# Kernel optimization log

Measured on AMD Instinct MI355X. Metric: run time of the kernel, lower is better.

Reference implementation:

```python
import jax, jax.numpy as jnp
import numpy as np

L, B, D, H = 128, 4, 768, 300
NT, NR = 7, 12  # ner tags, relation types
EPS = 1e-5


def _cummax(v):
    # torch: cumsum(softmax(v, -1), -1)
    return jnp.cumsum(jax.nn.softmax(v, axis=-1), axis=-1)


def _layernorm(v, g, b):
    mu = jnp.mean(v, axis=-1, keepdims=True)
    var = jnp.var(v, axis=-1, keepdims=True)
    return (v - mu) * jax.lax.rsqrt(var + EPS) * g + b


def setup_inputs() -> dict:
    key = jax.random.key(0)
    ks = jax.random.split(key, 24)
    s = lambda fan_in: 1.0 / np.sqrt(fan_in)
    u = lambda k, shape, sc: jax.random.uniform(k, shape, jnp.float32, -sc, sc)
    inp = {
        "x": jax.random.normal(ks[0], (L, B, D), jnp.float32),
        "mask": jnp.ones((L, B), jnp.float32),
        # PFN_Unit
        "W_ih": u(ks[1], (5 * H, D), s(D)), "b_ih": u(ks[2], (5 * H,), s(D)),
        "W_hh": u(ks[3], (5 * H, H), s(H)), "b_hh": u(ks[4], (5 * H,), s(H)),
        "W_tr": u(ks[5], (H, 3 * H), s(3 * H)), "b_tr": u(ks[6], (H,), s(3 * H)),
        # NERUnit
        "n_W": u(ks[7], (H, 2 * H), s(2 * H)), "n_b": u(ks[8], (H,), s(2 * H)),
        "ner_hW": u(ks[9], (H, 3 * H), s(3 * H)), "ner_hb": u(ks[10], (H,), s(3 * H)),
        "ner_g": jnp.ones((H,), jnp.float32), "ner_beta": jnp.zeros((H,), jnp.float32),
        "ner_tW": u(ks[11], (NT, H), s(H)), "ner_tb": u(ks[12], (NT,), s(H)),
        # ReUnit
        "r_W": u(ks[13], (H, 2 * H), s(2 * H)), "r_b": u(ks[14], (H,), s(2 * H)),
        "re_hW": u(ks[15], (H, 3 * H), s(3 * H)), "re_hb": u(ks[16], (H,), s(3 * H)),
        "re_g": jnp.ones((H,), jnp.float32), "re_beta": jnp.zeros((H,), jnp.float32),
        "re_tW": u(ks[17], (NR, H), s(H)), "re_tb": u(ks[18], (NR,), s(H)),
    }
    return inp


def _encoder(x, W_ih, b_ih, W_hh, b_hh, W_tr, b_tr):
    pre = jnp.einsum('lbd,gd->lbg', x, W_ih) + b_ih  # precompute input transform [L,B,5H]

    def step(carry, gx):
        h, c_in = carry
        gates = gx + h @ W_hh.T + b_hh
        c, eg_cin, rg_cin, eg_c, rg_c = jnp.split(gates, 5, axis=1)
        eg_cin, rg_cin = 1.0 - _cummax(eg_cin), _cummax(rg_cin)
        eg_c, rg_c = 1.0 - _cummax(eg_c), _cummax(rg_c)
        c = jnp.tanh(c)
        ov_c = rg_c * eg_c
        up_c, dn_c = rg_c - ov_c, eg_c - ov_c
        ov_i = rg_cin * eg_cin
        up_i, dn_i = rg_cin - ov_i, eg_cin - ov_i
        share = ov_i * c_in + ov_c * c
        c_re = up_i * c_in + up_c * c + share
        c_ner = dn_i * c_in + dn_c * c + share
        c_out = jnp.concatenate([c_re, c_ner, share], axis=-1) @ W_tr.T + b_tr
        h_out = jnp.tanh(c_out)
        return (h_out, c_out), (jnp.tanh(c_ner), jnp.tanh(c_re), jnp.tanh(share))

    h0 = jnp.zeros((x.shape[1], W_hh.shape[1]), x.dtype)
    _, (h_ner, h_re, h_share) = jax.lax.scan(step, (h0, h0), pre)
    return h_ner, h_re, h_share  # each [L,B,H]


def _pair_unit(h_task, h_share, mask, gW, gb, hW, hb, ln_g, ln_b, tW, tb, diag):
    length = h_task.shape[0]
    # global feature: tanh(Linear(cat(share, task))), max over time
    h_glob = jnp.tanh(jnp.concatenate([h_share, h_task], axis=-1) @ gW.T + gb)  # [L,B,H]
    g = jnp.max(h_glob, axis=0)  # [B,H]
    # pairwise feature [L,L,B,3H] = cat(start, end, global)
    st = jnp.broadcast_to(h_task[:, None], (length, length) + h_task.shape[1:])
    en = jnp.broadcast_to(h_task[None, :], (length, length) + h_task.shape[1:])
    gb4 = jnp.broadcast_to(g, (length, length) + g.shape)
    feat = jnp.concatenate([st, en, gb4], axis=-1)
    out = _layernorm(feat @ hW.T + hb, ln_g, ln_b)
    out = jax.nn.elu(out)  # eval mode: dropout is identity
    out = jax.nn.sigmoid(out @ tW.T + tb)  # [L,L,B,T]
    # mask
    m = mask[:, None, :] * mask[None, :, :]  # [L,L,B]
    if diag:
        m = m * jnp.triu(jnp.ones((length, length), out.dtype))[:, :, None]
    return out * m[..., None]


def reference(x, mask, W_ih, b_ih, W_hh, b_hh, W_tr, b_tr,
              n_W, n_b, ner_hW, ner_hb, ner_g, ner_beta, ner_tW, ner_tb,
              r_W, r_b, re_hW, re_hb, re_g, re_beta, re_tW, re_tb):
    h_ner, h_re, h_share = _encoder(x, W_ih, b_ih, W_hh, b_hh, W_tr, b_tr)
    ner = _pair_unit(h_ner, h_share, mask, n_W, n_b, ner_hW, ner_hb,
                     ner_g, ner_beta, ner_tW, ner_tb, diag=True)
    re = _pair_unit(h_re, h_share, mask, r_W, r_b, re_hW, re_hb,
                    re_g, re_beta, re_tW, re_tb, diag=False)
    return ner, re
```

## Files before the change

kernel.cpp:

```cpp
#include <hip/hip_runtime.h>

#define LLEN 128
#define BB 4
#define DD 768
#define HH 300
#define G5 1500
#define H3 900
#define NTT 7
#define NRR 12
#define NCHB 10
#define RPB 150
#define OPB 30

#define C_WIH  0
#define C_X    1152000
#define C_WHH2 1545216
#define C_WTR2 1995216
#define F_BIH  2265216
#define F_BTR  2266720
#define F_PRE  2267040
#define F_HG0  (F_PRE)
#define F_HG1  (F_PRE+153600)
#define F_A0   (F_PRE+307200)
#define F_E0   (F_PRE+460800)
#define F_GF0  (F_PRE+616832)
#define F_GF1  (F_PRE+618048)
#define F_HNER (F_PRE+768000)
#define F_HRE  (F_HNER+153600)
#define F_HSH  (F_HRE+153600)
#define F_A1   0
#define F_E1   153600
#define F_AUX  (F_HSH+153600)
#define AUXB   2432
#define AUX_FL 9728
#define WS_NEED_BYTES ((size_t)(F_AUX+11776)*4)

typedef unsigned short u16;
typedef unsigned int u32;
typedef float f4 __attribute__((ext_vector_type(4)));
typedef int i4 __attribute__((ext_vector_type(4)));

__device__ __forceinline__ float bf2f(u16 u) {
  union { u32 i; float f; } v; v.i = ((u32)u) << 16; return v.f;
}
__device__ __forceinline__ u16 f2bf(float f) {
  union { float f; u32 i; } v; v.f = f;
  u32 r = v.i + 0x7fffu + ((v.i >> 16) & 1u);
  return (u16)(r >> 16);
}
__device__ __forceinline__ float ldin(const void* p, int i, bool f32) {
  return f32 ? ((const float*)p)[i] : bf2f(((const u16*)p)[i]);
}
__device__ __forceinline__ bool is32(const void* mk) {
  return ((const u16*)mk)[0] == 0;
}
__device__ __forceinline__ float wsum(float x) {
  #pragma unroll
  for (int d = 1; d < 64; d <<= 1) x += __shfl_xor(x, d);
  return x;
}
__device__ __forceinline__ void astore(float* p, float v) {
  union { float f; int i; } u; u.f = v;
  __hip_atomic_store((int*)p, u.i, __ATOMIC_RELAXED, __HIP_MEMORY_SCOPE_AGENT);
}
__device__ __forceinline__ void gbar(int* flag, int tid, int target) {
  __syncthreads();
  if (tid == 0) {
    __builtin_amdgcn_s_waitcnt(0);
    __hip_atomic_fetch_add(flag, 1, __ATOMIC_RELAXED, __HIP_MEMORY_SCOPE_AGENT);
    int it = 0;
    while (__hip_atomic_load(flag, __ATOMIC_RELAXED, __HIP_MEMORY_SCOPE_AGENT) < target) {
      __builtin_amdgcn_s_sleep(1);
      if (++it > 50000) break;
    }
  }
  __syncthreads();
}
__device__ __forceinline__ f4 ld4x(const f4* p, int mode) {
  f4 v;
  if (mode)
    asm volatile("global_load_dwordx4 %0, %1, off sc0\n\ts_waitcnt vmcnt(0)"
                 : "=v"(v) : "v"(p) : "memory");
  else
    asm volatile("global_load_dwordx4 %0, %1, off sc0 sc1\n\ts_waitcnt vmcnt(0)"
                 : "=v"(v) : "v"(p) : "memory");
  return v;
}
__device__ __forceinline__ float ld1x(const float* p, int mode) {
  float v;
  if (mode)
    asm volatile("global_load_dword %0, %1, off sc0\n\ts_waitcnt vmcnt(0)"
                 : "=v"(v) : "v"(p) : "memory");
  else
    asm volatile("global_load_dword %0, %1, off sc0 sc1\n\ts_waitcnt vmcnt(0)"
                 : "=v"(v) : "v"(p) : "memory");
  return v;
}
__device__ __forceinline__ int ldix(const int* p, int mode) {
  int v;
  if (mode)
    asm volatile("global_load_dword %0, %1, off sc0\n\ts_waitcnt vmcnt(0)"
                 : "=v"(v) : "v"(p) : "memory");
  else
    asm volatile("global_load_dword %0, %1, off sc0 sc1\n\ts_waitcnt vmcnt(0)"
                 : "=v"(v) : "v"(p) : "memory");
  return v;
}
__device__ __forceinline__ void exst(float* p, float v, int mode) {
  if (mode) *p = v; else astore(p, v);
}
__device__ __forceinline__ int poll10(const int* slots, int tok, int mode) {
  i4 a, b, c;
  if (mode)
    asm volatile("global_load_dwordx4 %0, %3, off sc0\n\t"
                 "global_load_dwordx4 %1, %4, off sc0\n\t"
                 "global_load_dwordx4 %2, %5, off sc0\n\t"
                 "s_waitcnt vmcnt(0)"
                 : "=&v"(a), "=&v"(b), "=&v"(c)
                 : "v"(slots), "v"(slots + 4), "v"(slots + 8) : "memory");
  else
    asm volatile("global_load_dwordx4 %0, %3, off sc0 sc1\n\t"
                 "global_load_dwordx4 %1, %4, off sc0 sc1\n\t"
                 "global_load_dwordx4 %2, %5, off sc0 sc1\n\t"
                 "s_waitcnt vmcnt(0)"
                 : "=&v"(a), "=&v"(b), "=&v"(c)
                 : "v"(slots), "v"(slots + 4), "v"(slots + 8) : "memory");
  return (a.x >= tok) & (a.y >= tok) & (a.z >= tok) & (a.w >= tok) &
         (b.x >= tok) & (b.y >= tok) & (b.z >= tok) & (b.w >= tok) &
         (c.x >= tok) & (c.y >= tok);
}
__device__ __forceinline__ void sbar(int* slots, int ch, int tok, int tid, int mode) {
  asm volatile("s_waitcnt vmcnt(0)" ::: "memory");
  __syncthreads();
  if (tid == 0) {
    if (mode) slots[ch] = tok;
    else __hip_atomic_store(slots + ch, tok, __ATOMIC_RELAXED, __HIP_MEMORY_SCOPE_AGENT);
  }
  if (tid < 64) {
    int it = 0;
    while (!poll10(slots, tok, mode)) {
      __builtin_amdgcn_s_sleep(1);
      if (++it > 5000) break;
    }
  }
  __syncthreads();
}
__device__ __forceinline__ int claim_bc(int* cl, int nb) {
  unsigned xcd;
  asm volatile("s_getreg_b32 %0, hwreg(HW_REG_XCC_ID)" : "=s"(xcd));
  xcd &= 7u;
  int rank = __hip_atomic_fetch_add(cl + xcd, 1, __ATOMIC_RELAXED, __HIP_MEMORY_SCOPE_AGENT);
  __hip_atomic_fetch_add(cl + 8, 1, __ATOMIC_RELAXED, __HIP_MEMORY_SCOPE_AGENT);
  int it = 0;
  while (__hip_atomic_load(cl + 8, __ATOMIC_RELAXED, __HIP_MEMORY_SCOPE_AGENT) < nb) {
    __builtin_amdgcn_s_sleep(2);
    if (++it > 100000) break;
  }
  int base = 0;
  for (unsigned x = 0; x < xcd; ++x)
    base += __hip_atomic_load(cl + x, __ATOMIC_RELAXED, __HIP_MEMORY_SCOPE_AGENT) / NCHB;
  int cnt = __hip_atomic_load(cl + xcd, __ATOMIC_RELAXED, __HIP_MEMORY_SCOPE_AGENT);
  int slot = base + rank / NCHB;
  return (rank < (cnt / NCHB) * NCHB && slot < BB) ? (slot * 16 + rank % NCHB) : -1;
}

__global__ void k_canon(const void* xo, const void* mk, const void* Wih, const void* bih,
                        const void* Whh, const void* bhh, const void* Wtr, const void* btr,
                        float* ws) {
  bool f32 = is32(mk);
  int piece = blockIdx.y;
  int i = blockIdx.x * 256 + threadIdx.x;
  switch (piece) {
    case 0: if (!f32 && i < 1152000) ws[C_WIH + i] = ldin(Wih, i, f32); break;
    case 1: if (!f32 && i < 393216)  ws[C_X + i]   = ldin(xo, i, f32);  break;
    case 2: if (i < 225000) {
      int k2 = i / G5, out = i - k2 * G5;
      float2 v;
      v.x = ldin(Whh, out * HH + 2 * k2, f32);
      v.y = ldin(Whh, out * HH + 2 * k2 + 1, f32);
      ((float2*)(ws + C_WHH2))[i] = v;
    } break;
    case 3: if (i < 135000) {
      int k2 = i / HH, out = i - k2 * HH;
      float2 v;
      v.x = ldin(Wtr, out * H3 + 2 * k2, f32);
      v.y = ldin(Wtr, out * H3 + 2 * k2 + 1, f32);
      ((float2*)(ws + C_WTR2))[i] = v;
    } break;
    case 4: {
      if (i < 1504) ws[F_BIH + i] = (i < G5) ? ldin(bih, i, f32) + ldin(bhh, i, f32) : 0.f;
      else if (i < 1824) { int j = i - 1504; ws[F_BTR + j] = (j < HH) ? ldin(btr, j, f32) : 0.f; }
    } break;
    case 5: if (i < 11776) ws[F_AUX + i] = 0.f; break;
  }
}

__global__ void k_pre2(const void* xo, const void* Wo, const void* mk,
                       const float* cX, const float* cW, const float* biasf, float* pre) {
  bool f32 = is32(mk);
  const float* X = f32 ? (const float*)xo : cX;
  const float* W = f32 ? (const float*)Wo : cW;
  __shared__ __align__(16) float xl[8 * DD];
  int tid = threadIdx.x;
  int lb0 = (blockIdx.x >> 1) * 8;
  int half = blockIdx.x & 1;
  for (int e = tid; e < 8 * DD; e += 256) xl[e] = X[(size_t)lb0 * DD + e];
  __syncthreads();
  for (int j = half * 750 + tid; j < half * 750 + 750; j += 256) {
    const float4* w = (const float4*)(W + (size_t)j * DD);
    float acc[8] = {0.f, 0.f, 0.f, 0.f, 0.f, 0.f, 0.f, 0.f};
    #pragma unroll 2
    for (int k = 0; k < DD / 4; ++k) {
      float4 u = w[k];
      #pragma unroll
      for (int r = 0; r < 8; ++r) {
        const float4 p = *(const float4*)(xl + r * DD + k * 4);
        acc[r] += u.x * p.x + u.y * p.y + u.z * p.z + u.w * p.w;
      }
    }
    float bias = biasf[j];
    #pragma unroll
    for (int r = 0; r < 8; ++r) pre[(size_t)(lb0 + r) * G5 + j] = acc[r] + bias;
  }
}

__global__ void __launch_bounds__(512, 2) k_scan8(const float* pre, const float2* W2h, const float2* W2t,
                                                  const float* btrf, float* hner, float* hre, float* hsh,
                                                  float* aux) {
  __shared__ __align__(16) float h_l[304];
  __shared__ __align__(16) float ci_l[304];
  __shared__ __align__(16) float ga_l[1504];
  __shared__ __align__(16) float cat_l[904];
  __shared__ __align__(16) float ps[512];
  __shared__ __align__(16) float sums_l[8];
  __shared__ float exv[160];
  __shared__ int s_bc, s_mode;
  int tid = threadIdx.x;
  int* ibase = (int*)(aux + AUX_FL);
  if (tid == 0) s_bc = claim_bc(ibase, (int)gridDim.x);
  __syncthreads();
  int bc = s_bc;
  if (bc < 0) return;
  int b = bc >> 4, ch = bc & 15;
  int s = ch >> 1;
  int r0 = ch * RPB;
  float* gb   = aux + b * AUXB;
  float* cb   = gb + 1504;
  float* hb   = gb + 1808;
  float* sums = gb + 2112;
  int* slotsA = ibase + 32 + b * 64;
  int* slotsB = slotsA + 16;
  int* atf    = slotsA + 32;

  {
    float* tst = gb + 2176;
    int* seflag = (int*)(gb + 2208);
    if (ch == 0 && tid == 0) tst[0] = 1.0f;
    gbar(atf + 0, tid, NCHB);
    if (tid == 0) { float w1 = ld1x(tst, 1); (void)w1; }
    gbar(atf + 1, tid, NCHB);
    if (ch == 0 && tid == 0) { tst[0] = 2.0f; __builtin_amdgcn_s_waitcnt(0); }
    if (ch == 1 && tid == 0)
      __hip_atomic_fetch_add(seflag, 1, __ATOMIC_RELAXED, __HIP_MEMORY_SCOPE_WORKGROUP);
    gbar(atf + 2, tid, NCHB);
    if (tid == 0) {
      float w2 = ld1x(tst, 1);
      int fv = ldix(seflag, 1);
      if (w2 != 2.0f || fv != 1)
        __hip_atomic_fetch_or(atf + 4, 1, __ATOMIC_RELAXED, __HIP_MEMORY_SCOPE_AGENT);
    }
    gbar(atf + 3, tid, NCHB);
    if (tid == 0)
      s_mode = (__hip_atomic_load(atf + 4, __ATOMIC_RELAXED, __HIP_MEMORY_SCOPE_AGENT) == 0) ? 1 : 0;
    __syncthreads();
  }
  int mode = s_mode;

  int j = tid / RPB, r = tid - j * RPB;
  int o2 = tid % OPB, jj = tid / OPB;
  int kb = j * 100;

  float2 wh[50];
  if (tid < 450) {
    const float2* wp = W2h + (size_t)(j * 50) * G5 + (r0 + r);
    #pragma unroll
    for (int kk = 0; kk < 50; ++kk) wh[kk] = wp[(size_t)kk * G5];
  }
  float2 wt[29];
  int k2b = jj * 29;
  int k2e = (k2b + 29 < 450) ? (k2b + 29) : 450;
  int nk2 = k2e - k2b;
  if (tid < 480) {
    const float2* wp = W2t + (size_t)k2b * HH + (ch * OPB + o2);
    #pragma unroll
    for (int q = 0; q < 29; ++q) if (q < nk2) wt[q] = wp[(size_t)q * HH];
  }
  float pv = 0.f;
  if (tid < RPB) pv = pre[(size_t)b * G5 + r0 + tid];
  __syncthreads();

  for (int t = 0; t < LLEN; ++t) {
    if (t > 0) {
      if (tid < 75)       { f4 v = ld4x((const f4*)hb + tid, mode); *(f4*)(h_l + 4 * tid) = v; }
      else if (tid < 150) { int q = tid - 75; f4 v = ld4x((const f4*)cb + q, mode); *(f4*)(ci_l + 4 * q) = v; }
      __syncthreads();
    }
    if (tid < 450) {
      float acc = (j == 0) ? pv : 0.f;
      if (t > 0) {
        #pragma unroll
        for (int kk = 0; kk < 50; ++kk)
          acc += wh[kk].x * h_l[kb + 2 * kk] + wh[kk].y * h_l[kb + 2 * kk + 1];
      }
      ps[tid] = acc;
    }
    __syncthreads();
    if (tid < RPB) {
      float g = ps[tid] + ps[RPB + tid] + ps[2 * RPB + tid];
      if (s == 0) exst(gb + r0 + tid, tanhf(g), mode);
      else exv[tid] = __expf(g);
    }
    if (s > 0) {
      __syncthreads();
      if (tid < 30) {
        int base2 = tid * 5;
        float e0 = exv[base2], e1 = exv[base2 + 1], e2 = exv[base2 + 2],
              e3 = exv[base2 + 3], e4 = exv[base2 + 4];
        float p = ((e0 + e1) + (e2 + e3)) + e4;
        float inc = p;
        #pragma unroll
        for (int d = 1; d < 32; d <<= 1) { float o = __shfl_up(inc, d); if (tid >= d) inc += o; }
        float tot = __shfl(inc, 29);
        float run = inc - p;
        run += e0; exst(gb + r0 + base2,     run, mode);
        run += e1; exst(gb + r0 + base2 + 1, run, mode);
        run += e2; exst(gb + r0 + base2 + 2, run, mode);
        run += e3; exst(gb + r0 + base2 + 3, run, mode);
        run += e4; exst(gb + r0 + base2 + 4, run, mode);
        if (tid == 0) exst(sums + (ch - 2), tot, mode);
      }
    }
    sbar(slotsA, ch, t + 1, tid, mode);
    if (tid < 375)      { f4 v = ld4x((const f4*)gb + tid, mode); *(f4*)(ga_l + 4 * tid) = v; }
    else if (tid < 377) { int q = tid - 375; f4 v = ld4x((const f4*)sums + q, mode); *(f4*)(sums_l + 4 * q) = v; }
    float pvn = 0.f;
    if (t + 1 < LLEN && tid < RPB) pvn = pre[((size_t)(t + 1) * BB + b) * G5 + r0 + tid];
    __syncthreads();
    if (tid < HH) {
      float c = ga_l[tid];
      float v[4];
      #pragma unroll
      for (int s1 = 0; s1 < 4; ++s1) {
        float raw = ga_l[(s1 + 1) * HH + tid];
        float off = (tid >= RPB) ? sums_l[2 * s1] : 0.f;
        float S = sums_l[2 * s1] + sums_l[2 * s1 + 1];
        v[s1] = (raw + off) / S;
      }
      float eg_cin = 1.f - v[0], rg_cin = v[1], eg_c = 1.f - v[2], rg_c = v[3];
      float ci = (t > 0) ? ci_l[tid] : 0.f;
      float ov_c = rg_c * eg_c;
      float up_c = rg_c - ov_c, dn_c = eg_c - ov_c;
      float ov_i = rg_cin * eg_cin;
      float up_i = rg_cin - ov_i, dn_i = eg_cin - ov_i;
      float share = ov_i * ci + ov_c * c;
      float c_re  = up_i * ci + up_c * c + share;
      float c_ner = dn_i * ci + dn_c * c + share;
      cat_l[tid] = c_re; cat_l[HH + tid] = c_ner; cat_l[2 * HH + tid] = share;
      int sb = ch * OPB;
      if (tid >= sb && tid < sb + OPB) {
        size_t ob = ((size_t)t * BB + b) * HH + tid;
        hner[ob] = tanhf(c_ner); hre[ob] = tanhf(c_re); hsh[ob] = tanhf(share);
      }
    }
    __syncthreads();
    if (tid < 480) {
      float acc = 0.f;
      #pragma unroll
      for (int q = 0; q < 29; ++q)
        if (q < nk2) acc += wt[q].x * cat_l[2 * (k2b + q)] + wt[q].y * cat_l[2 * (k2b + q) + 1];
      ps[tid] = acc;
    }
    __syncthreads();
    if (tid < OPB) {
      float co = btrf[ch * OPB + tid];
      #pragma unroll
      for (int q = 0; q < 16; ++q) co += ps[q * OPB + tid];
      exst(cb + ch * OPB + tid, co, mode);
      exst(hb + ch * OPB + tid, tanhf(co), mode);
    }
    if (t + 1 < LLEN) sbar(slotsB, ch, t + 1, tid, mode);
    pv = pvn;
  }
}

__global__ void k_glob3(const float* hsh, const float* hner, const float* hre,
                        const void* nW, const void* nb, const void* rW, const void* rb,
                        const void* mk, float* hg0, float* hg1) {
  bool f32 = is32(mk);
  int task = blockIdx.x >> 7;
  int lb0 = (blockIdx.x & 127) * 4;
  const float* tsk = task ? hre : hner;
  const void* gWo = task ? rW : nW;
  const void* gbo = task ? rb : nb;
  float* hg = task ? hg1 : hg0;
  __shared__ __align__(16) float catl[2400];
  int tid = threadIdx.x;
  for (int e = tid; e < 2400; e += 320) {
    int rr = e / 600, c = e - rr * 600;
    catl[e] = (c < HH) ? hsh[(size_t)(lb0 + rr) * HH + c] : tsk[(size_t)(lb0 + rr) * HH + (c - HH)];
  }
  __syncthreads();
  if (tid < HH) {
    float bias = ldin(gbo, tid, f32);
    float acc[4] = {bias, bias, bias, bias};
    if (f32) {
      const float4* row = (const float4*)((const float*)gWo + (size_t)tid * 600);
      #pragma unroll 2
      for (int k = 0; k < 150; ++k) {
        float4 u = row[k];
        #pragma unroll
        for (int rr = 0; rr < 4; ++rr) {
          const float4 cv = *(const float4*)(catl + rr * 600 + 4 * k);
          acc[rr] += u.x * cv.x + u.y * cv.y + u.z * cv.z + u.w * cv.w;
        }
      }
    } else {
      for (int k = 0; k < 600; ++k) {
        float w = ldin(gWo, tid * 600 + k, f32);
        #pragma unroll
        for (int rr = 0; rr < 4; ++rr) acc[rr] += w * catl[rr * 600 + k];
      }
    }
    #pragma unroll
    for (int rr = 0; rr < 4; ++rr) hg[(size_t)(lb0 + rr) * HH + tid] = tanhf(acc[rr]);
  }
}

__global__ void k_feat2(const float* hner, const float* hre,
                        const void* nhW, const void* nhb, const void* rhW, const void* rhb,
                        const void* mk, float* A0, float* E0, float* A1, float* E1) {
  bool f32 = is32(mk);
  int task = blockIdx.x >> 7;
  int lb0 = (blockIdx.x & 127) * 4;
  const float* tsk = task ? hre : hner;
  const void* hWo = task ? rhW : nhW;
  const void* hbo = task ? rhb : nhb;
  float* A = task ? A1 : A0;
  float* E = task ? E1 : E0;
  __shared__ __align__(16) float tl[1200];
  int tid = threadIdx.x;
  for (int e = tid; e < 1200; e += 320) {
    int rr = e / 300, c = e - rr * 300;
    tl[e] = tsk[(size_t)(lb0 + rr) * HH + c];
  }
  __syncthreads();
  if (tid < HH) {
    float bias = ldin(hbo, tid, f32);
    float a[4] = {bias, bias, bias, bias};
    float ev[4] = {0.f, 0.f, 0.f, 0.f};
    if (f32) {
      const float4* r1 = (const float4*)((const float*)hWo + (size_t)tid * H3);
      const float4* r2 = (const float4*)((const float*)hWo + (size_t)tid * H3 + HH);
      #pragma unroll 2
      for (int k = 0; k < 75; ++k) {
        float4 u = r1[k], w2 = r2[k];
        #pragma unroll
        for (int rr = 0; rr < 4; ++rr) {
          const float4 tv = *(const float4*)(tl + rr * 300 + 4 * k);
          a[rr]  += u.x * tv.x + u.y * tv.y + u.z * tv.z + u.w * tv.w;
          ev[rr] += w2.x * tv.x + w2.y * tv.y + w2.z * tv.z + w2.w * tv.w;
        }
      }
    } else {
      for (int k = 0; k < HH; ++k) {
        float w1 = ldin(hWo, tid * H3 + k, f32);
        float w2 = ldin(hWo, tid * H3 + HH + k, f32);
        #pragma unroll
        for (int rr = 0; rr < 4; ++rr) {
          a[rr] += w1 * tl[rr * 300 + k];
          ev[rr] += w2 * tl[rr * 300 + k];
        }
      }
    }
    #pragma unroll
    for (int rr = 0; rr < 4; ++rr) {
      A[(size_t)(lb0 + rr) * HH + tid] = a[rr];
      E[(size_t)(lb0 + rr) * HH + tid] = ev[rr];
    }
  }
}

__global__ void k_gmf(const float* hg0, const float* hg1, const void* nhW, const void* rhW,
                      const void* mk, float* Gf0, float* Gf1) {
  bool f32 = is32(mk);
  int task = blockIdx.x >> 2, b = blockIdx.x & 3;
  const float* hg = task ? hg1 : hg0;
  const void* hWo = task ? rhW : nhW;
  float* Gf = task ? Gf1 : Gf0;
  __shared__ __align__(16) float gl[304];
  int tid = threadIdx.x;
  if (tid < HH) {
    float m = -1e30f;
    for (int l = 0; l < LLEN; ++l) m = fmaxf(m, hg[((size_t)l * BB + b) * HH + tid]);
    gl[tid] = m;
  }
  __syncthreads();
  if (tid < HH) {
    float acc = 0.f;
    if (f32) {
      const float4* row = (const float4*)((const float*)hWo + (size_t)tid * H3 + 600);
      #pragma unroll 5
      for (int k = 0; k < 75; ++k) {
        float4 u = row[k];
        const float4 gv = *(const float4*)(gl + 4 * k);
        acc += u.x * gv.x + u.y * gv.y + u.z * gv.z + u.w * gv.w;
      }
    } else {
      for (int k = 0; k < HH; ++k) acc += gl[k] * ldin(hWo, tid * H3 + 600 + k, f32);
    }
    Gf[b * HH + tid] = acc;
  }
}

__global__ void __launch_bounds__(256) k_pair6(const float* A0, const float* E0, const float* Gf0,
                                               const void* lg0, const void* lb0_, const void* tW0, const void* tb0,
                                               const float* A1, const float* E1, const float* Gf1,
                                               const void* lg1, const void* lb1_, const void* tW1, const void* tb1,
                                               const void* mk, void* outv) {
  __shared__ float lg_l[304], lb_l[304], tb_l[16];
  __shared__ float tw_l[3616];
  bool f32 = is32(mk);
  int tau = blockIdx.x >> 12;
  int bid = blockIdx.x & 4095;
  const float* A  = tau ? A1 : A0;
  const float* E  = tau ? E1 : E0;
  const float* Gf = tau ? Gf1 : Gf0;
  const void* lgo = tau ? lg1 : lg0;
  const void* lbo = tau ? lb1_ : lb0_;
  const void* tWo = tau ? tW1 : tW0;
  const void* tbo = tau ? tb1 : tb0;
  int T = tau ? NRR : NTT;
  int diag = tau ? 0 : 1;
  int Toff = tau ? 458752 : 0;
  int tid = threadIdx.x;
  for (int i2 = tid; i2 < HH; i2 += 256) { lg_l[i2] = ldin(lgo, i2, f32); lb_l[i2] = ldin(lbo, i2, f32); }
  for (int i2 = tid; i2 < T * HH; i2 += 256) tw_l[i2] = ldin(tWo, i2, f32);
  if (tid < T) tb_l[tid] = ldin(tbo, tid, f32);
  __syncthreads();
  int i = bid >> 5;
  int j0 = (bid & 31) << 2;
  int b = tid >> 6, ln = tid & 63;
  const float* ar = A  + (size_t)(i * BB + b) * HH;
  const float* gr = Gf + (size_t)b * HH;
  bool ok4 = ln < 44;
  float a0 = ar[ln]       + gr[ln];
  float a1 = ar[64 + ln]  + gr[64 + ln];
  float a2 = ar[128 + ln] + gr[128 + ln];
  float a3 = ar[192 + ln] + gr[192 + ln];
  float a4 = ok4 ? (ar[256 + ln] + gr[256 + ln]) : 0.f;
  float mi = ldin(mk, i * BB + b, f32);
  for (int dj = 0; dj < 4; ++dj) {
    int jx = j0 + dj;
    const float* er = E + (size_t)(jx * BB + b) * HH;
    float u0 = a0 + er[ln];
    float u1 = a1 + er[64 + ln];
    float u2 = a2 + er[128 + ln];
    float u3 = a3 + er[192 + ln];
    float u4 = ok4 ? (a4 + er[256 + ln]) : 0.f;
    float s1 = ((u0 + u1) + (u2 + u3)) + u4;
    float s2 = ((u0 * u0 + u1 * u1) + (u2 * u2 + u3 * u3)) + u4 * u4;
    #pragma unroll
    for (int d = 1; d < 64; d <<= 1) { s1 += __shfl_xor(s1, d); s2 += __shfl_xor(s2, d); }
    float mean = s1 * (1.f / 300.f);
    float var = s2 * (1.f / 300.f) - mean * mean;
    float rstd = rsqrtf(var + 1e-5f);
    {
      float y;
      y = (u0 - mean) * rstd * lg_l[ln]       + lb_l[ln];       u0 = (y > 0.f) ? y : __expf(y) - 1.f;
      y = (u1 - mean) * rstd * lg_l[64 + ln]  + lb_l[64 + ln];  u1 = (y > 0.f) ? y : __expf(y) - 1.f;
      y = (u2 - mean) * rstd * lg_l[128 + ln] + lb_l[128 + ln]; u2 = (y > 0.f) ? y : __expf(y) - 1.f;
      y = (u3 - mean) * rstd * lg_l[192 + ln] + lb_l[192 + ln]; u3 = (y > 0.f) ? y : __expf(y) - 1.f;
      if (ok4) {
        y = (u4 - mean) * rstd * lg_l[256 + ln] + lb_l[256 + ln];
        u4 = (y > 0.f) ? y : __expf(y) - 1.f;
      }
    }
    float m = mi * ldin(mk, jx * BB + b, f32);
    if (diag && jx < i) m = 0.f;
    size_t obase = (size_t)Toff + ((size_t)(i * LLEN + jx) * BB + b) * T;
    float mine = 0.f;
    for (int t = 0; t < T; ++t) {
      const float* twr = tw_l + t * HH;
      float s = u0 * twr[ln] + u1 * twr[64 + ln] + u2 * twr[128 + ln] + u3 * twr[192 + ln];
      if (ok4) s += u4 * twr[256 + ln];
      s = wsum(s);
      s += tb_l[t];
      float o = m / (1.f + __expf(-s));
      mine = (ln == t) ? o : mine;
    }
    if (ln < T) {
      if (f32) ((float*)outv)[obase + ln] = mine;
      else ((u16*)outv)[obase + ln] = f2bf(mine);
    }
  }
}

__global__ void k_sent(const void* mk, const void* xo, void* outv, int hostcode) {
  __shared__ int bad;
  if (threadIdx.x == 0) bad = 0;
  __syncthreads();
  bool f32 = is32(mk);
  for (int i = threadIdx.x; i < 4096; i += 256) {
    float v = ldin(xo, i, f32);
    if (!(v == v) || fabsf(v) > 1e6f) bad = 1;
  }
  __syncthreads();
  if (threadIdx.x == 0) {
    float code = (float)hostcode;
    if (bad) code = fmaxf(code, 88.f);
    if (code > 0.f) {
      if (f32) ((float*)outv)[0] = code;
      else ((u16*)outv)[0] = f2bf(code);
    }
  }
}

extern "C" void kernel_launch(void* const* d_in, const int* in_sizes, int n_in,
                              void* d_out, int out_size, void* d_ws, size_t ws_size,
                              hipStream_t stream) {
  const void* x    = d_in[0];
  const void* mask = d_in[1];
  const void* Wih  = d_in[2];
  const void* bih  = d_in[3];
  const void* Whh  = d_in[4];
  const void* bhh  = d_in[5];
  const void* Wtr  = d_in[6];
  const void* btr  = d_in[7];
  const void* nW   = d_in[8];
  const void* nb   = d_in[9];
  const void* nhW  = d_in[10];
  const void* nhb  = d_in[11];
  const void* ng   = d_in[12];
  const void* nbe  = d_in[13];
  const void* ntW  = d_in[14];
  const void* ntb  = d_in[15];
  const void* rW   = d_in[16];
  const void* rb   = d_in[17];
  const void* rhW  = d_in[18];
  const void* rhb  = d_in[19];
  const void* rg   = d_in[20];
  const void* rbe  = d_in[21];
  const void* rtW  = d_in[22];
  const void* rtb  = d_in[23];
  float* ws = (float*)d_ws;

  static const int exp_sz[24] = {393216, 512, 1152000, 1500, 450000, 1500, 270000, 300,
                                 180000, 300, 270000, 300, 300, 300, 2100, 7,
                                 180000, 300, 270000, 300, 300, 300, 3600, 12};
  int hostcode = 0;
  if (n_in != 24) hostcode = 890;
  else {
    for (int ii = 0; ii < 24; ++ii)
      if (in_sizes[ii] != exp_sz[ii]) { hostcode = 900 + ii; break; }
  }
  if (hostcode == 0 && out_size != 1245184) hostcode = 880;
  if (hostcode == 0 && ws_size < WS_NEED_BYTES) hostcode = 1099;

  dim3 gc(4500, 6);
  k_canon<<<gc, 256, 0, stream>>>(x, mask, Wih, bih, Whh, bhh, Wtr, btr, ws);
  k_pre2<<<128, 256, 0, stream>>>(x, Wih, mask, ws + C_X, ws + C_WIH, ws + F_BIH, ws + F_PRE);
  k_scan8<<<256, 512, 0, stream>>>(ws + F_PRE, (const float2*)(ws + C_WHH2), (const float2*)(ws + C_WTR2),
                                   ws + F_BTR, ws + F_HNER, ws + F_HRE, ws + F_HSH, ws + F_AUX);
  k_glob3<<<256, 320, 0, stream>>>(ws + F_HSH, ws + F_HNER, ws + F_HRE,
                                   nW, nb, rW, rb, mask, ws + F_HG0, ws + F_HG1);
  k_feat2<<<256, 320, 0, stream>>>(ws + F_HNER, ws + F_HRE, nhW, nhb, rhW, rhb, mask,
                                   ws + F_A0, ws + F_E0, ws + F_A1, ws + F_E1);
  k_gmf<<<8, 320, 0, stream>>>(ws + F_HG0, ws + F_HG1, nhW, rhW, mask, ws + F_GF0, ws + F_GF1);
  k_pair6<<<8192, 256, 0, stream>>>(ws + F_A0, ws + F_E0, ws + F_GF0, ng, nbe, ntW, ntb,
                                    ws + F_A1, ws + F_E1, ws + F_GF1, rg, rbe, rtW, rtb,
                                    mask, d_out);
  k_sent<<<1, 256, 0, stream>>>(mask, x, d_out, hostcode);
}
```

Baseline: 1.471 ms.

## Restructure scan recurrence to one cross-block barrier per step with K-split partials

The recurrent scan kernel now splits the h@W_hh product along the hidden (K) dimension rather than by output rows. Each of the 10 blocks per batch uses its own 30-element slice of h, kept in shared memory, to compute partial sums for all 1500 gate outputs and writes them to a double-buffered global scratch area. After a single inter-block barrier, every block reads back and reduces the partials, then computes tanh and the cumulative softmaxes locally and redundantly. This drops the second per-step grid barrier and the separate exchange of gates and sums, at the cost of more global partial-sum traffic per step and duplicated gate math in every block. It reuses the start of the workspace (the canonical W_ih region) as scratch, which is only safe if that data is no longer needed after the pre-projection kernel.

Result: slower. 2.154 ms (+46.4%).

```diff
diff --git a/kernel.cpp b/kernel.cpp
--- a/kernel.cpp
+++ b/kernel.cpp
@@ -31,6 +31,7 @@
 #define F_A1   0
 #define F_E1   153600
 #define F_AUX  (F_HSH+153600)
+#define P_CPUB 192000
 #define AUXB   2432
 #define AUX_FL 9728
 #define WS_NEED_BYTES ((size_t)(F_AUX+11776)*4)
@@ -108,6 +109,40 @@
 }
 __device__ __forceinline__ void exst(float* p, float v, int mode) {
   if (mode) *p = v; else astore(p, v);
+}
+__device__ __forceinline__ void ld9(const float* base, int mode,
+                                    f4& a0, f4& a1, f4& a2, f4& a3, f4& a4,
+                                    f4& a5, f4& a6, f4& a7, f4& a8) {
+  if (mode)
+    asm volatile(
+      "global_load_dwordx4 %0, %9, off sc0\n\t"
+      "global_load_dwordx4 %1, %9, off offset:16 sc0\n\t"
+      "global_load_dwordx4 %2, %9, off offset:32 sc0\n\t"
+      "global_load_dwordx4 %3, %9, off offset:64 sc0\n\t"
+      "global_load_dwordx4 %4, %9, off offset:80 sc0\n\t"
+      "global_load_dwordx4 %5, %9, off offset:96 sc0\n\t"
+      "global_load_dwordx4 %6, %9, off offset:128 sc0\n\t"
+      "global_load_dwordx4 %7, %9, off offset:144 sc0\n\t"
+      "global_load_dwordx4 %8, %9, off offset:160 sc0\n\t"
+      "s_waitcnt vmcnt(0)"
+      : "=&v"(a0), "=&v"(a1), "=&v"(a2), "=&v"(a3), "=&v"(a4),
+        "=&v"(a5), "=&v"(a6), "=&v"(a7), "=&v"(a8)
+      : "v"(base) : "memory");
+  else
+    asm volatile(
+      "global_load_dwordx4 %0, %9, off sc0 sc1\n\t"
+      "global_load_dwordx4 %1, %9, off offset:16 sc0 sc1\n\t"
+      "global_load_dwordx4 %2, %9, off offset:32 sc0 sc1\n\t"
+      "global_load_dwordx4 %3, %9, off offset:64 sc0 sc1\n\t"
+      "global_load_dwordx4 %4, %9, off offset:80 sc0 sc1\n\t"
+      "global_load_dwordx4 %5, %9, off offset:96 sc0 sc1\n\t"
+      "global_load_dwordx4 %6, %9, off offset:128 sc0 sc1\n\t"
+      "global_load_dwordx4 %7, %9, off offset:144 sc0 sc1\n\t"
+      "global_load_dwordx4 %8, %9, off offset:160 sc0 sc1\n\t"
+      "s_waitcnt vmcnt(0)"
+      : "=&v"(a0), "=&v"(a1), "=&v"(a2), "=&v"(a3), "=&v"(a4),
+        "=&v"(a5), "=&v"(a6), "=&v"(a7), "=&v"(a8)
+      : "v"(base) : "memory");
 }
 __device__ __forceinline__ int poll10(const int* slots, int tok, int mode) {
   i4 a, b, c;
@@ -224,16 +259,16 @@
   }
 }
 
-__global__ void __launch_bounds__(512, 2) k_scan8(const float* pre, const float2* W2h, const float2* W2t,
+__global__ void __launch_bounds__(512, 2) k_scan9(const float* pre, const float2* W2h, const float2* W2t,
                                                   const float* btrf, float* hner, float* hre, float* hsh,
-                                                  float* aux) {
-  __shared__ __align__(16) float h_l[304];
+                                                  float* aux, float* xw) {
+  __shared__ __align__(16) float ga_l[1504];
+  __shared__ __align__(16) float vv_l[1204];
+  __shared__ __align__(16) float tnh_l[304];
+  __shared__ __align__(16) float cat_l[904];
   __shared__ __align__(16) float ci_l[304];
-  __shared__ __align__(16) float ga_l[1504];
-  __shared__ __align__(16) float cat_l[904];
   __shared__ __align__(16) float ps[512];
-  __shared__ __align__(16) float sums_l[8];
-  __shared__ float exv[160];
+  __shared__ __align__(16) float h_loc[32];
   __shared__ int s_bc, s_mode;
   int tid = threadIdx.x;
   int* ibase = (int*)(aux + AUX_FL);
@@ -242,14 +277,8 @@
   int bc = s_bc;
   if (bc < 0) return;
   int b = bc >> 4, ch = bc & 15;
-  int s = ch >> 1;
-  int r0 = ch * RPB;
-  float* gb   = aux + b * AUXB;
-  float* cb   = gb + 1504;
-  float* hb   = gb + 1808;
-  float* sums = gb + 2112;
+  float* gb = aux + b * AUXB;
   int* slotsA = ibase + 32 + b * 64;
-  int* slotsB = slotsA + 16;
   int* atf    = slotsA + 32;
 
   {
@@ -276,16 +305,24 @@
   }
   int mode = s_mode;
 
-  int j = tid / RPB, r = tid - j * RPB;
+  if (ch < 2) {
+    float* pb0 = xw + (size_t)ch * 96000 + b * 24000;
+    for (int i = tid; i < 3000; i += 512) {
+      int row = i >> 1, col = 10 + (i & 1);
+      exst(pb0 + row * 16 + col, 0.f, mode);
+    }
+  }
+
+  int o0 = 3 * tid;
+  float2 wh2[45];
+  if (tid < 500) {
+    #pragma unroll
+    for (int j = 0; j < 3; ++j)
+      #pragma unroll
+      for (int kk = 0; kk < 15; ++kk)
+        wh2[j * 15 + kk] = W2h[(size_t)(ch * 15 + kk) * G5 + (o0 + j)];
+  }
   int o2 = tid % OPB, jj = tid / OPB;
-  int kb = j * 100;
-
-  float2 wh[50];
-  if (tid < 450) {
-    const float2* wp = W2h + (size_t)(j * 50) * G5 + (r0 + r);
-    #pragma unroll
-    for (int kk = 0; kk < 50; ++kk) wh[kk] = wp[(size_t)kk * G5];
-  }
   float2 wt[29];
   int k2b = jj * 29;
   int k2e = (k2b + 29 < 450) ? (k2b + 29) : 450;
@@ -295,68 +332,91 @@
     #pragma unroll
     for (int q = 0; q < 29; ++q) if (q < nk2) wt[q] = wp[(size_t)q * HH];
   }
-  float pv = 0.f;
-  if (tid < RPB) pv = pre[(size_t)b * G5 + r0 + tid];
+  float pv0 = 0.f, pv1 = 0.f, pv2 = 0.f;
+  if (tid < 500) {
+    const float* pr = pre + (size_t)b * G5 + o0;
+    pv0 = pr[0]; pv1 = pr[1]; pv2 = pr[2];
+  }
   __syncthreads();
 
   for (int t = 0; t < LLEN; ++t) {
+    int buf = t & 1;
+    float* pb = xw + (size_t)buf * 96000 + b * 24000;
     if (t > 0) {
-      if (tid < 75)       { f4 v = ld4x((const f4*)hb + tid, mode); *(f4*)(h_l + 4 * tid) = v; }
-      else if (tid < 150) { int q = tid - 75; f4 v = ld4x((const f4*)cb + q, mode); *(f4*)(ci_l + 4 * q) = v; }
-      __syncthreads();
-    }
-    if (tid < 450) {
-      float acc = (j == 0) ? pv : 0.f;
-      if (t > 0) {
+      if (tid < 500) {
+        float2 h2[15];
         #pragma unroll
-        for (int kk = 0; kk < 50; ++kk)
-          acc += wh[kk].x * h_l[kb + 2 * kk] + wh[kk].y * h_l[kb + 2 * kk + 1];
-      }
-      ps[tid] = acc;
+        for (int kk = 0; kk < 15; ++kk) h2[kk] = *(const float2*)(h_loc + 2 * kk);
+        #pragma unroll
+        for (int j = 0; j < 3; ++j) {
+          float acc = 0.f;
+          #pragma unroll
+          for (int kk = 0; kk < 15; ++kk)
+            acc += wh2[j * 15 + kk].x * h2[kk].x + wh2[j * 15 + kk].y * h2[kk].y;
+          exst(pb + (size_t)(o0 + j) * 16 + ch, acc, mode);
+        }
+      }
+      sbar(slotsA, ch, t, tid, mode);
+      if (tid < 500) {
+        f4 a0, a1, a2, a3, a4, a5, a6, a7, a8;
+        ld9(pb + (size_t)o0 * 16, mode, a0, a1, a2, a3, a4, a5, a6, a7, a8);
+        ga_l[o0]     = pv0 + (((a0.x + a0.y) + (a0.z + a0.w)) +
+                              ((a1.x + a1.y) + (a1.z + a1.w)) +
+                              ((a2.x + a2.y) + (a2.z + a2.w)));
+        ga_l[o0 + 1] = pv1 + (((a3.x + a3.y) + (a3.z + a3.w)) +
+                              ((a4.x + a4.y) + (a4.z + a4.w)) +
+                              ((a5.x + a5.y) + (a5.z + a5.w)));
+        ga_l[o0 + 2] = pv2 + (((a6.x + a6.y) + (a6.z + a6.w)) +
+                              ((a7.x + a7.y) + (a7.z + a7.w)) +
+                              ((a8.x + a8.y) + (a8.z + a8.w)));
+      }
+      if (tid < 75) {
+        const float* cp = xw + P_CPUB + (size_t)(((t - 1) & 1) * 4 + b) * 304;
+        f4 v = ld4x((const f4*)cp + tid, mode);
+        *(f4*)(ci_l + 4 * tid) = v;
+      }
+    } else {
+      if (tid < 500) { ga_l[o0] = pv0; ga_l[o0 + 1] = pv1; ga_l[o0 + 2] = pv2; }
     }
     __syncthreads();
-    if (tid < RPB) {
-      float g = ps[tid] + ps[RPB + tid] + ps[2 * RPB + tid];
-      if (s == 0) exst(gb + r0 + tid, tanhf(g), mode);
-      else exv[tid] = __expf(g);
-    }
-    if (s > 0) {
-      __syncthreads();
-      if (tid < 30) {
-        int base2 = tid * 5;
-        float e0 = exv[base2], e1 = exv[base2 + 1], e2 = exv[base2 + 2],
-              e3 = exv[base2 + 3], e4 = exv[base2 + 4];
-        float p = ((e0 + e1) + (e2 + e3)) + e4;
+    if (tid < HH) tnh_l[tid] = tanhf(ga_l[tid]);
+    {
+      int w = tid >> 6, ln = tid & 63;
+      if (w >= 4) {
+        int c = w - 3;
+        const float* g = ga_l + c * 300;
+        int e0 = ln * 5;
+        float ex0 = 0.f, ex1 = 0.f, ex2 = 0.f, ex3 = 0.f, ex4 = 0.f;
+        if (ln < 60) {
+          ex0 = __expf(g[e0]); ex1 = __expf(g[e0 + 1]); ex2 = __expf(g[e0 + 2]);
+          ex3 = __expf(g[e0 + 3]); ex4 = __expf(g[e0 + 4]);
+        }
+        float p = ((ex0 + ex1) + (ex2 + ex3)) + ex4;
         float inc = p;
         #pragma unroll
-        for (int d = 1; d < 32; d <<= 1) { float o = __shfl_up(inc, d); if (tid >= d) inc += o; }
-        float tot = __shfl(inc, 29);
+        for (int d = 1; d < 64; d <<= 1) { float o = __shfl_up(inc, d); if (ln >= d) inc += o; }
+        float S = __shfl(inc, 59);
+        float invS = 1.f / S;
         float run = inc - p;
-        run += e0; exst(gb + r0 + base2,     run, mode);
-        run += e1; exst(gb + r0 + base2 + 1, run, mode);
-        run += e2; exst(gb + r0 + base2 + 2, run, mode);
-        run += e3; exst(gb + r0 + base2 + 3, run, mode);
-        run += e4; exst(gb + r0 + base2 + 4, run, mode);
-        if (tid == 0) exst(sums + (ch - 2), tot, mode);
-      }
-    }
-    sbar(slotsA, ch, t + 1, tid, mode);
-    if (tid < 375)      { f4 v = ld4x((const f4*)gb + tid, mode); *(f4*)(ga_l + 4 * tid) = v; }
-    else if (tid < 377) { int q = tid - 375; f4 v = ld4x((const f4*)sums + q, mode); *(f4*)(sums_l + 4 * q) = v; }
-    float pvn = 0.f;
-    if (t + 1 < LLEN && tid < RPB) pvn = pre[((size_t)(t + 1) * BB + b) * G5 + r0 + tid];
+        if (ln < 60) {
+          float* vv = vv_l + (c - 1) * 300 + e0;
+          run += ex0; vv[0] = run * invS;
+          run += ex1; vv[1] = run * invS;
+          run += ex2; vv[2] = run * invS;
+          run += ex3; vv[3] = run * invS;
+          run += ex4; vv[4] = run * invS;
+        }
+      }
+    }
+    if (t + 1 < LLEN && tid < 500) {
+      const float* pr = pre + ((size_t)(t + 1) * BB + b) * G5 + o0;
+      pv0 = pr[0]; pv1 = pr[1]; pv2 = pr[2];
+    }
     __syncthreads();
     if (tid < HH) {
-      float c = ga_l[tid];
-      float v[4];
-      #pragma unroll
-      for (int s1 = 0; s1 < 4; ++s1) {
-        float raw = ga_l[(s1 + 1) * HH + tid];
-        float off = (tid >= RPB) ? sums_l[2 * s1] : 0.f;
-        float S = sums_l[2 * s1] + sums_l[2 * s1 + 1];
-        v[s1] = (raw + off) / S;
-      }
-      float eg_cin = 1.f - v[0], rg_cin = v[1], eg_c = 1.f - v[2], rg_c = v[3];
+      float c = tnh_l[tid];
+      float v0 = vv_l[tid], v1 = vv_l[300 + tid], v2 = vv_l[600 + tid], v3 = vv_l[900 + tid];
+      float eg_cin = 1.f - v0, rg_cin = v1, eg_c = 1.f - v2, rg_c = v3;
       float ci = (t > 0) ? ci_l[tid] : 0.f;
       float ov_c = rg_c * eg_c;
       float up_c = rg_c - ov_c, dn_c = eg_c - ov_c;
@@ -385,11 +445,11 @@
       float co = btrf[ch * OPB + tid];
       #pragma unroll
       for (int q = 0; q < 16; ++q) co += ps[q * OPB + tid];
-      exst(cb + ch * OPB + tid, co, mode);
-      exst(hb + ch * OPB + tid, tanhf(co), mode);
-    }
-    if (t + 1 < LLEN) sbar(slotsB, ch, t + 1, tid, mode);
-    pv = pvn;
+      h_loc[tid] = tanhf(co);
+      float* cp = xw + P_CPUB + (size_t)(buf * 4 + b) * 304;
+      exst(cp + ch * OPB + tid, co, mode);
+    }
+    __syncthreads();
   }
 }
 
@@ -669,8 +729,8 @@
   dim3 gc(4500, 6);
   k_canon<<<gc, 256, 0, stream>>>(x, mask, Wih, bih, Whh, bhh, Wtr, btr, ws);
   k_pre2<<<128, 256, 0, stream>>>(x, Wih, mask, ws + C_X, ws + C_WIH, ws + F_BIH, ws + F_PRE);
-  k_scan8<<<256, 512, 0, stream>>>(ws + F_PRE, (const float2*)(ws + C_WHH2), (const float2*)(ws + C_WTR2),
-                                   ws + F_BTR, ws + F_HNER, ws + F_HRE, ws + F_HSH, ws + F_AUX);
+  k_scan9<<<256, 512, 0, stream>>>(ws + F_PRE, (const float2*)(ws + C_WHH2), (const float2*)(ws + C_WTR2),
+                                   ws + F_BTR, ws + F_HNER, ws + F_HRE, ws + F_HSH, ws + F_AUX, ws);
   k_glob3<<<256, 320, 0, stream>>>(ws + F_HSH, ws + F_HNER, ws + F_HRE,
                                    nW, nb, rW, rb, mask, ws + F_HG0, ws + F_HG1);
   k_feat2<<<256, 320, 0, stream>>>(ws + F_HNER, ws + F_HRE, nhW, nhb, rhW, rhb, mask,
```
